# Optimization experiments

Hardware: AMD Instinct MI355X
Metric: run time of the kernel (lower is better)

## Reference

```python
import jax, jax.numpy as jnp
import numpy as np

B, T, C, H = 32, 576, 1024, 16
D = C // H  # head_dim = 64

def setup_inputs() -> dict:
    key = jax.random.key(0)
    ks = jax.random.split(key, 5)
    s = 1.0 / np.sqrt(C)
    return {
        "emb_img": jax.random.normal(ks[0], (B, T, C), dtype=jnp.float32),
        "w_qkv": jax.random.normal(ks[1], (C, 3 * C), dtype=jnp.float32) * s,
        "b_qkv": jnp.zeros((3 * C,), dtype=jnp.float32),
        "w_proj": jax.random.normal(ks[2], (C, C), dtype=jnp.float32) * s,
        "b_proj": jnp.zeros((C,), dtype=jnp.float32),
    }

def reference(emb_img, w_qkv, b_qkv, w_proj, b_proj):
    # fused QKV projection
    qkv = emb_img @ w_qkv + b_qkv                       # [B,T,3C]
    q, k, v = jnp.split(qkv, 3, axis=-1)                # each [B,T,C]
    def heads(x):
        return x.reshape(B, T, H, D).transpose(0, 2, 1, 3)  # [B,H,T,D]
    q, k, v = heads(q), heads(k), heads(v)
    # note: original scales by 1/head_dim (not 1/sqrt(head_dim))
    scores = jnp.einsum("bhqd,bhkd->bhqk", q, k) * (1.0 / D)
    causal = jnp.tril(jnp.ones((T, T), dtype=bool))
    scores = jnp.where(causal[None, None], scores, -jnp.inf)
    att = jax.nn.softmax(scores, axis=-1)               # [B,H,T,T]
    y = jnp.einsum("bhqk,bhkd->bhqd", att, v)           # [B,H,T,D]
    y = y.transpose(0, 2, 1, 3).reshape(B, T, C)
    return y @ w_proj + b_proj
```

## Files before the change

kernel.cpp:

```cpp
#include <hip/hip_runtime.h>
#include <stdint.h>

namespace {

constexpr int kB = 32, kT = 576, kC = 1024, kH = 16, kD = 64;
constexpr int kM = kB * kT;
constexpr int kNqkv = 3 * kC;
constexpr float kQScale = 1.4426950408889634f / 64.0f;

typedef uint16_t u16;
typedef __attribute__((ext_vector_type(4))) float f32x4;
typedef __attribute__((ext_vector_type(8))) short short8;
typedef __attribute__((ext_vector_type(8))) __bf16 bf16x8;
typedef __attribute__((ext_vector_type(4))) uint16_t u16x4;

#define VMCNT(n) asm volatile("s_waitcnt vmcnt(" #n ")" ::: "memory")

__device__ __forceinline__ float fexp2(float x) {
  return __builtin_amdgcn_exp2f(x);
}

__device__ __forceinline__ f32x4 mfma_bf16(short8 a, short8 b, f32x4 c) {
  return __builtin_amdgcn_mfma_f32_16x16x32_bf16(
      __builtin_bit_cast(bf16x8, a), __builtin_bit_cast(bf16x8, b), c, 0, 0, 0);
}

__device__ __forceinline__ u16 to_bf16(float x) {
  uint32_t u = __float_as_uint(x);
  u += 0x7fffu + ((u >> 16) & 1u);
  return (u16)(u >> 16);
}

__device__ __forceinline__ void gload_lds16(const void* g, void* l) {
  __builtin_amdgcn_global_load_lds(
      (const __attribute__((address_space(1))) uint32_t*)(uintptr_t)g,
      (__attribute__((address_space(3))) uint32_t*)(uintptr_t)l,
      16, 0, 0);
}

__device__ __forceinline__ void bar() {
  asm volatile("" ::: "memory");
  __builtin_amdgcn_s_barrier();
  asm volatile("" ::: "memory");
}

__global__ __launch_bounds__(256) void cvt_bf16_kernel(
    const float* __restrict__ in, u16* __restrict__ out, int n4) {
  const int i = blockIdx.x * 256 + threadIdx.x;
  if (i >= n4) return;
  const f32x4 v = ((const f32x4*)in)[i];
  u16x4 o;
#pragma unroll
  for (int j = 0; j < 4; ++j) o[j] = to_bf16(v[j]);
  ((u16x4*)out)[i] = o;
}

__global__ void tconv_kernel(const float* __restrict__ in, u16* __restrict__ out,
                             int K, int N) {
  __shared__ u16 tile[32][33];
  const int nb = blockIdx.x * 32;
  const int kb = blockIdx.y * 32;
  const int tx = threadIdx.x;
  const int ty = threadIdx.y;
#pragma unroll
  for (int i = 0; i < 32; i += 8)
    tile[ty + i][tx] = to_bf16(in[(size_t)(kb + ty + i) * N + nb + tx]);
  __syncthreads();
#pragma unroll
  for (int i = 0; i < 32; i += 8)
    out[(size_t)(nb + ty + i) * K + kb + tx] = tile[tx][ty + i];
}

__global__ __launch_bounds__(512, 4) void gemm_qkv(
    const u16* __restrict__ A, const u16* __restrict__ Bt,
    const float* __restrict__ bias,
    u16* __restrict__ outQ, u16* __restrict__ outK, u16* __restrict__ outVT) {
  constexpr int Kc = 1024;
  constexpr int NT = Kc / 32;
  __shared__ char lds[2][24576];

  const int tid = threadIdx.x;
  const int wave = tid >> 6;
  const int lane = tid & 63;
  const int lo = lane & 15;
  const int hi = lane >> 4;
  const int wr = wave >> 1;
  const int wc = wave & 1;

  const int lin = blockIdx.x + blockIdx.y * 24;
  const int l2 = (lin & 7) * 216 + (lin >> 3);
  const int n0 = (l2 % 24) * 128;
  const int m0 = (l2 / 24) * 256;

  const u16* srcA[2];
#pragma unroll
  for (int c = 0; c < 2; ++c) {
    const int off = c * 8192 + tid * 16;
    const int p = off >> 7;
    const int col = (off & 127) ^ ((p & 7) << 4);
    const int Ar = (col < 64) ? p : p + 128;
    const int k_ = (col & 63) >> 1;
    srcA[c] = A + (size_t)(m0 + Ar) * Kc + k_;
  }
  const u16* srcB1;
  {
    const int off = tid * 16;
    const int p = off >> 7;
    const int col = (off & 127) ^ ((p & 7) << 4);
    const int Br = (col < 64) ? p : p + 64;
    const int k_ = (col & 63) >> 1;
    srcB1 = Bt + (size_t)(n0 + Br) * Kc + k_;
  }

  auto stage = [&](int slot, int t) {
    char* base = &lds[slot][0];
    gload_lds16(srcA[0] + t * 32, base + tid * 16);
    gload_lds16(srcA[1] + t * 32, base + 8192 + tid * 16);
    gload_lds16(srcB1 + t * 32, base + 16384 + tid * 16);
  };

  f32x4 acc[4][4] = {};

  auto compute = [&](int slot) {
    const char* base = &lds[slot][0];
    const char* baseB = base + 16384;
    const int swz = (lo & 7) << 4;
    short8 af[4], bf[4];
#pragma unroll
    for (int i = 0; i < 4; ++i) {
      const int row = wr * 64 + i * 16 + lo;
      const int prow = row & 127;
      const int half = row >> 7;
      af[i] = *(const short8*)(base + prow * 128 + ((half * 64 + hi * 16) ^ swz));
    }
#pragma unroll
    for (int j = 0; j < 4; ++j) {
      const int row = wc * 64 + j * 16 + lo;
      const int prow = row & 63;
      const int half = row >> 6;
      bf[j] = *(const short8*)(baseB + prow * 128 + ((half * 64 + hi * 16) ^ swz));
    }
    __builtin_amdgcn_s_setprio(1);
#pragma unroll
    for (int i = 0; i < 4; ++i)
#pragma unroll
      for (int j = 0; j < 4; ++j)
        acc[i][j] = mfma_bf16(af[i], bf[j], acc[i][j]);
    __builtin_amdgcn_s_setprio(0);
  };

  stage(0, 0);
  for (int t = 0; t < NT; ++t) {
    if (t + 1 < NT) {
      stage((t + 1) & 1, t + 1);
      VMCNT(3);
    } else {
      VMCNT(0);
    }
    bar();
    compute(t & 1);
    bar();
  }

  if (n0 >= 2048) {
    u16* wlds = (u16*)&lds[0][0] + wave * (32 * 66);
    uint32_t* wlds32 = (uint32_t*)wlds;
#pragma unroll
    for (int jp = 0; jp < 2; ++jp) {
#pragma unroll
      for (int jj = 0; jj < 2; ++jj) {
        const int j = jp * 2 + jj;
        const int n = n0 + wc * 64 + j * 16 + lo;
        const float bv = bias[n];
        const int dl = jj * 16 + lo;
#pragma unroll
        for (int i = 0; i < 4; ++i)
#pragma unroll
          for (int rp = 0; rp < 2; ++rp) {
            const u16 w0 = to_bf16(acc[i][j][rp * 2] + bv);
            const u16 w1 = to_bf16(acc[i][j][rp * 2 + 1] + bv);
            wlds32[dl * 33 + i * 8 + hi * 2 + rp] =
                (uint32_t)w0 | ((uint32_t)w1 << 16);
          }
      }
#pragma unroll
      for (int p = 0; p < 8; ++p) {
        const int dl32 = p * 4 + hi;
        const int n = n0 + wc * 64 + jp * 32 + dl32;
        const int c = n & 1023;
        const int hh = c >> 6;
        const int d = c & 63;
        const int m = m0 + wr * 64 + lo * 4;
        const int bb = m / kT;
        const int t = m - bb * kT;
        const u16x4 v = *(const u16x4*)&wlds[dl32 * 66 + lo * 4];
        *(u16x4*)&outVT[((size_t)(bb * kH + hh) * kD + d) * kT + t] = v;
      }
    }
  } else {
#pragma unroll
    for (int j = 0; j < 4; ++j) {
      const int n = n0 + wc * 64 + j * 16 + lo;
      const float bv = bias[n];
      const int which = n >> 10;
      const int c = n & 1023;
      const int hh = c >> 6;
      const int d = c & 63;
#pragma unroll
      for (int i = 0; i < 4; ++i) {
        const int mrow = m0 + wr * 64 + i * 16 + hi * 4;
#pragma unroll
        for (int r = 0; r < 4; ++r) {
          const int m = mrow + r;
          const int bb = m / kT;
          const int t = m - bb * kT;
          const float v = acc[i][j][r] + bv;
          if (which == 0)
            outQ[((size_t)(bb * kH + hh) * kT + t) * kD + d] = to_bf16(v * kQScale);
          else
            outK[((size_t)(bb * kH + hh) * kT + t) * kD + d] = to_bf16(v);
        }
      }
    }
  }
}

__global__ __launch_bounds__(256, 3) void gemm_proj(
    const u16* __restrict__ A, const u16* __restrict__ Bt,
    const float* __restrict__ bias, float* __restrict__ outF) {
  constexpr int Kc = 1024;
  constexpr int NT = Kc / 32;
  __shared__ char lds[3][16384];

  const int tid = threadIdx.x;
  const int wave = tid >> 6;
  const int lane = tid & 63;
  const int lo = lane & 15;
  const int hi = lane >> 4;
  const int wr = wave >> 1;
  const int wc = wave & 1;

  const int lin = blockIdx.x + blockIdx.y * 8;
  const int l2 = (lin & 7) * 144 + (lin >> 3);
  const int n0 = (l2 & 7) * 128;
  const int m0 = (l2 >> 3) * 128;

  const u16* srcA[2];
  const u16* srcB[2];
#pragma unroll
  for (int c = 0; c < 2; ++c) {
    const int off = c * 4096 + tid * 16;
    const int p = off >> 7;
    const int col = (off & 127) ^ ((p & 7) << 4);
    const int r_ = (col < 64) ? p : p + 64;
    const int k_ = (col & 63) >> 1;
    srcA[c] = A + (size_t)(m0 + r_) * Kc + k_;
    srcB[c] = Bt + (size_t)(n0 + r_) * Kc + k_;
  }

  auto stage = [&](int slot, int t) {
    char* base = &lds[slot][0];
#pragma unroll
    for (int c = 0; c < 2; ++c) {
      gload_lds16(srcA[c] + t * 32, base + c * 4096 + wave * 1024);
      gload_lds16(srcB[c] + t * 32, base + 8192 + c * 4096 + wave * 1024);
    }
  };

  f32x4 acc[4][4] = {};

  auto compute = [&](int slot) {
    const char* base = &lds[slot][0];
    const char* baseB = base + 8192;
    const int swz = (lo & 7) << 4;
    short8 af[4], bf[4];
#pragma unroll
    for (int i = 0; i < 4; ++i)
      af[i] = *(const short8*)(base + (i * 16 + lo) * 128 + ((wr * 64 + hi * 16) ^ swz));
#pragma unroll
    for (int j = 0; j < 4; ++j)
      bf[j] = *(const short8*)(baseB + (j * 16 + lo) * 128 + ((wc * 64 + hi * 16) ^ swz));
    __builtin_amdgcn_s_setprio(1);
#pragma unroll
    for (int i = 0; i < 4; ++i)
#pragma unroll
      for (int j = 0; j < 4; ++j)
        acc[i][j] = mfma_bf16(af[i], bf[j], acc[i][j]);
    __builtin_amdgcn_s_setprio(0);
  };

  stage(0, 0);
  stage(1, 1);
  for (int t = 0; t < NT - 2; ++t) {
    stage((t + 2) % 3, t + 2);
    VMCNT(8);
    bar();
    compute(t % 3);
    bar();
  }
  VMCNT(4);
  bar();
  compute((NT - 2) % 3);
  bar();
  VMCNT(0);
  bar();
  compute((NT - 1) % 3);

#pragma unroll
  for (int j = 0; j < 4; ++j) {
    const int n = n0 + wc * 64 + j * 16 + lo;
    const float bv = bias[n];
#pragma unroll
    for (int i = 0; i < 4; ++i) {
      const int mrow = m0 + wr * 64 + i * 16 + hi * 4;
#pragma unroll
      for (int r = 0; r < 4; ++r)
        outF[(size_t)(mrow + r) * kC + n] = acc[i][j][r] + bv;
    }
  }
}

__global__ __launch_bounds__(256) void attn_kernel(
    const u16* __restrict__ Q, const u16* __restrict__ K,
    const u16* __restrict__ VT, u16* __restrict__ Y) {
  __shared__ u16 P[4][32][72];

  const int idx = blockIdx.x;
  const int qi = 4 - (idx >> 9);
  const int bh = idx & 511;
  const int wave = threadIdx.x >> 6;
  const int lane = threadIdx.x & 63;
  const int lo = lane & 15;
  const int hi = lane >> 4;
  const int q0 = qi * 128 + wave * 32;
  if (q0 >= kT) return;

  const u16* Qb = Q + (size_t)bh * kT * kD;
  const u16* Kb = K + (size_t)bh * kT * kD;
  const u16* Vb = VT + (size_t)bh * kD * kT;

  short8 qf[2][2];
#pragma unroll
  for (int h = 0; h < 2; ++h) {
    const u16* qp = Qb + (q0 + h * 16 + lo) * kD + hi * 8;
    qf[h][0] = *(const short8*)qp;
    qf[h][1] = *(const short8*)(qp + 32);
  }

  f32x4 acc[2][4] = {};
  float mrun[2] = {-3e38f, -3e38f};
  float lsum[2] = {0.f, 0.f};

  short8 kf[4][2];
#pragma unroll
  for (int kc = 0; kc < 4; ++kc) {
    const u16* kp = Kb + (kc * 16 + lo) * kD + hi * 8;
    kf[kc][0] = *(const short8*)kp;
    kf[kc][1] = *(const short8*)(kp + 32);
  }

  const int kv_end = q0 + 32;
  for (int kv = 0; kv < kv_end; kv += 64) {
    f32x4 s[2][4];
#pragma unroll
    for (int kc = 0; kc < 4; ++kc)
#pragma unroll
      for (int h = 0; h < 2; ++h) {
        f32x4 z = {0.f, 0.f, 0.f, 0.f};
        z = mfma_bf16(kf[kc][0], qf[h][0], z);
        z = mfma_bf16(kf[kc][1], qf[h][1], z);
        s[h][kc] = z;
      }
    short8 vf[4][2];
#pragma unroll
    for (int nt = 0; nt < 4; ++nt) {
      const u16* vp = Vb + (nt * 16 + lo) * kT + kv + hi * 8;
      vf[nt][0] = *(const short8*)vp;
      vf[nt][1] = *(const short8*)(vp + 32);
    }
    if (kv + 64 < kv_end) {
#pragma unroll
      for (int kc = 0; kc < 4; ++kc) {
        const u16* kp = Kb + (kv + 64 + kc * 16 + lo) * kD + hi * 8;
        kf[kc][0] = *(const short8*)kp;
        kf[kc][1] = *(const short8*)(kp + 32);
      }
    }
    if (kv + 63 > q0) {
#pragma unroll
      for (int h = 0; h < 2; ++h) {
        const int q = q0 + h * 16 + lo;
#pragma unroll
        for (int kc = 0; kc < 4; ++kc)
#pragma unroll
          for (int r = 0; r < 4; ++r)
            if (kv + kc * 16 + hi * 4 + r > q) s[h][kc][r] = -3e38f;
      }
    }
#pragma unroll
    for (int h = 0; h < 2; ++h) {
      float m01 = fmaxf(fmaxf(s[h][0][0], s[h][0][1]), fmaxf(s[h][0][2], s[h][0][3]));
      float m23 = fmaxf(fmaxf(s[h][1][0], s[h][1][1]), fmaxf(s[h][1][2], s[h][1][3]));
      float m45 = fmaxf(fmaxf(s[h][2][0], s[h][2][1]), fmaxf(s[h][2][2], s[h][2][3]));
      float m67 = fmaxf(fmaxf(s[h][3][0], s[h][3][1]), fmaxf(s[h][3][2], s[h][3][3]));
      float pm = fmaxf(fmaxf(m01, m23), fmaxf(m45, m67));
      pm = fmaxf(pm, __shfl_xor(pm, 16));
      pm = fmaxf(pm, __shfl_xor(pm, 32));
      const float mnew = fmaxf(mrun[h], pm);
      const float corr = fexp2(mrun[h] - mnew);
      mrun[h] = mnew;
      float psum = 0.f;
#pragma unroll
      for (int kc = 0; kc < 4; ++kc) {
        u16x4 pk;
#pragma unroll
        for (int r = 0; r < 4; ++r) {
          const float pv = fexp2(s[h][kc][r] - mnew);
          psum += pv;
          pk[r] = to_bf16(pv);
        }
        *(u16x4*)&P[wave][h * 16 + lo][kc * 16 + hi * 4] = pk;
      }
      lsum[h] = lsum[h] * corr + psum;
#pragma unroll
      for (int nt = 0; nt < 4; ++nt)
#pragma unroll
        for (int r = 0; r < 4; ++r) acc[h][nt][r] *= corr;
    }
    short8 pf[2][2];
#pragma unroll
    for (int h = 0; h < 2; ++h) {
      pf[h][0] = *(const short8*)&P[wave][h * 16 + lo][hi * 8];
      pf[h][1] = *(const short8*)&P[wave][h * 16 + lo][32 + hi * 8];
    }
#pragma unroll
    for (int nt = 0; nt < 4; ++nt)
#pragma unroll
      for (int h = 0; h < 2; ++h) {
        acc[h][nt] = mfma_bf16(pf[h][0], vf[nt][0], acc[h][nt]);
        acc[h][nt] = mfma_bf16(pf[h][1], vf[nt][1], acc[h][nt]);
      }
  }

#pragma unroll
  for (int h = 0; h < 2; ++h) {
    lsum[h] += __shfl_xor(lsum[h], 16);
    lsum[h] += __shfl_xor(lsum[h], 32);
  }
  const int b = bh >> 4, hh = bh & 15;
#pragma unroll
  for (int h = 0; h < 2; ++h)
#pragma unroll
    for (int r = 0; r < 4; ++r) {
      const float linv = 1.0f / __shfl(lsum[h], hi * 4 + r);
      const int t = q0 + h * 16 + hi * 4 + r;
      const size_t base = ((size_t)(b * kT + t) * kH + hh) * kD;
#pragma unroll
      for (int nt = 0; nt < 4; ++nt)
        Y[base + nt * 16 + lo] = to_bf16(acc[h][nt][r] * linv);
    }
}

}

extern "C" void kernel_launch(void* const* d_in, const int* in_sizes, int n_in,
                              void* d_out, int out_size, void* d_ws, size_t ws_size,
                              hipStream_t stream) {
  (void)in_sizes; (void)n_in; (void)out_size; (void)ws_size;
  const float* emb   = (const float*)d_in[0];
  const float* wqkv  = (const float*)d_in[1];
  const float* bqkv  = (const float*)d_in[2];
  const float* wproj = (const float*)d_in[3];
  const float* bproj = (const float*)d_in[4];
  float* out = (float*)d_out;

  char* p = (char*)d_ws;
  u16* embb   = (u16*)p; p += (size_t)kM * kC * 2;
  u16* wqkvt  = (u16*)p; p += (size_t)kNqkv * kC * 2;
  u16* wprojt = (u16*)p; p += (size_t)kC * kC * 2;
  u16* Qh     = (u16*)p; p += (size_t)kM * kC * 2;
  u16* Kh     = (u16*)p; p += (size_t)kM * kC * 2;
  u16* VTh    = (u16*)p; p += (size_t)kM * kC * 2;
  u16* Yh     = (u16*)p; p += (size_t)kM * kC * 2;

  const int n4 = kM * kC / 4;
  cvt_bf16_kernel<<<dim3((n4 + 255) / 256), 256, 0, stream>>>(emb, embb, n4);
  tconv_kernel<<<dim3(kNqkv / 32, kC / 32), dim3(32, 8), 0, stream>>>(wqkv, wqkvt, kC, kNqkv);
  tconv_kernel<<<dim3(kC / 32, kC / 32), dim3(32, 8), 0, stream>>>(wproj, wprojt, kC, kC);
  gemm_qkv<<<dim3(kNqkv / 128, kM / 256), 512, 0, stream>>>(
      embb, wqkvt, bqkv, Qh, Kh, VTh);
  attn_kernel<<<dim3(5 * kB * kH), 256, 0, stream>>>(Qh, Kh, VTh, Yh);
  gemm_proj<<<dim3(kC / 128, kM / 128), 256, 0, stream>>>(
      Yh, wprojt, bproj, out);
}
```

Baseline: 317.7 us.

## Enlarge proj GEMM tile to 256x128 and skip masked half-tiles in attention

The output projection GEMM now uses 512-thread blocks with 256x128 tiles, double-buffered LDS instead of triple-buffered, so each B tile is reused across twice as many rows. The attention kernel splits the KV loop into unmasked full tiles and one masked diagonal tile, and for the last tile it processes only the 32 needed keys when the query block ends mid-tile. This cuts wasted MFMA, exp and mask work on the causal diagonal. The cost is shallower pipelining in the GEMM and higher per-block register and LDS pressure.

```diff
diff --git a/kernel.cpp b/kernel.cpp
--- a/kernel.cpp
+++ b/kernel.cpp
@@ -225,12 +225,12 @@
   }
 }
 
-__global__ __launch_bounds__(256, 3) void gemm_proj(
+__global__ __launch_bounds__(512, 4) void gemm_proj(
     const u16* __restrict__ A, const u16* __restrict__ Bt,
     const float* __restrict__ bias, float* __restrict__ outF) {
   constexpr int Kc = 1024;
   constexpr int NT = Kc / 32;
-  __shared__ char lds[3][16384];
+  __shared__ char lds[2][24576];
 
   const int tid = threadIdx.x;
   const int wave = tid >> 6;
@@ -241,45 +241,58 @@
   const int wc = wave & 1;
 
   const int lin = blockIdx.x + blockIdx.y * 8;
-  const int l2 = (lin & 7) * 144 + (lin >> 3);
-  const int n0 = (l2 & 7) * 128;
-  const int m0 = (l2 >> 3) * 128;
+  const int l2 = (lin & 7) * 72 + (lin >> 3);
+  const int n0 = (l2 % 8) * 128;
+  const int m0 = (l2 / 8) * 256;
 
   const u16* srcA[2];
-  const u16* srcB[2];
 #pragma unroll
   for (int c = 0; c < 2; ++c) {
-    const int off = c * 4096 + tid * 16;
+    const int off = c * 8192 + tid * 16;
     const int p = off >> 7;
     const int col = (off & 127) ^ ((p & 7) << 4);
-    const int r_ = (col < 64) ? p : p + 64;
+    const int Ar = (col < 64) ? p : p + 128;
     const int k_ = (col & 63) >> 1;
-    srcA[c] = A + (size_t)(m0 + r_) * Kc + k_;
-    srcB[c] = Bt + (size_t)(n0 + r_) * Kc + k_;
+    srcA[c] = A + (size_t)(m0 + Ar) * Kc + k_;
+  }
+  const u16* srcB1;
+  {
+    const int off = tid * 16;
+    const int p = off >> 7;
+    const int col = (off & 127) ^ ((p & 7) << 4);
+    const int Br = (col < 64) ? p : p + 64;
+    const int k_ = (col & 63) >> 1;
+    srcB1 = Bt + (size_t)(n0 + Br) * Kc + k_;
   }
 
   auto stage = [&](int slot, int t) {
     char* base = &lds[slot][0];
-#pragma unroll
-    for (int c = 0; c < 2; ++c) {
-      gload_lds16(srcA[c] + t * 32, base + c * 4096 + wave * 1024);
-      gload_lds16(srcB[c] + t * 32, base + 8192 + c * 4096 + wave * 1024);
-    }
+    gload_lds16(srcA[0] + t * 32, base + tid * 16);
+    gload_lds16(srcA[1] + t * 32, base + 8192 + tid * 16);
+    gload_lds16(srcB1 + t * 32, base + 16384 + tid * 16);
   };
 
   f32x4 acc[4][4] = {};
 
   auto compute = [&](int slot) {
     const char* base = &lds[slot][0];
-    const char* baseB = base + 8192;
+    const char* baseB = base + 16384;
     const int swz = (lo & 7) << 4;
     short8 af[4], bf[4];
 #pragma unroll
-    for (int i = 0; i < 4; ++i)
-      af[i] = *(const short8*)(base + (i * 16 + lo) * 128 + ((wr * 64 + hi * 16) ^ swz));
-#pragma unroll
-    for (int j = 0; j < 4; ++j)
-      bf[j] = *(const short8*)(baseB + (j * 16 + lo) * 128 + ((wc * 64 + hi * 16) ^ swz));
+    for (int i = 0; i < 4; ++i) {
+      const int row = wr * 64 + i * 16 + lo;
+      const int prow = row & 127;
+      const int half = row >> 7;
+      af[i] = *(const short8*)(base + prow * 128 + ((half * 64 + hi * 16) ^ swz));
+    }
+#pragma unroll
+    for (int j = 0; j < 4; ++j) {
+      const int row = wc * 64 + j * 16 + lo;
+      const int prow = row & 63;
+      const int half = row >> 6;
+      bf[j] = *(const short8*)(baseB + prow * 128 + ((half * 64 + hi * 16) ^ swz));
+    }
     __builtin_amdgcn_s_setprio(1);
 #pragma unroll
     for (int i = 0; i < 4; ++i)
@@ -290,21 +303,17 @@
   };
 
   stage(0, 0);
-  stage(1, 1);
-  for (int t = 0; t < NT - 2; ++t) {
-    stage((t + 2) % 3, t + 2);
-    VMCNT(8);
+  for (int t = 0; t < NT; ++t) {
+    if (t + 1 < NT) {
+      stage((t + 1) & 1, t + 1);
+      VMCNT(3);
+    } else {
+      VMCNT(0);
+    }
     bar();
-    compute(t % 3);
+    compute(t & 1);
     bar();
   }
-  VMCNT(4);
-  bar();
-  compute((NT - 2) % 3);
-  bar();
-  VMCNT(0);
-  bar();
-  compute((NT - 1) % 3);
 
 #pragma unroll
   for (int j = 0; j < 4; ++j) {
@@ -359,51 +368,77 @@
     kf[kc][1] = *(const short8*)(kp + 32);
   }
 
-  const int kv_end = q0 + 32;
-  for (int kv = 0; kv < kv_end; kv += 64) {
+  const int nfull = q0 >> 6;
+  const bool tail4 = ((q0 >> 5) & 1) != 0;
+
+  auto do_tile = [&](int kv, int kclim, bool masked, bool have_next,
+                     bool next_wide) {
     f32x4 s[2][4];
 #pragma unroll
-    for (int kc = 0; kc < 4; ++kc)
-#pragma unroll
-      for (int h = 0; h < 2; ++h) {
-        f32x4 z = {0.f, 0.f, 0.f, 0.f};
-        z = mfma_bf16(kf[kc][0], qf[h][0], z);
-        z = mfma_bf16(kf[kc][1], qf[h][1], z);
-        s[h][kc] = z;
-      }
+    for (int kc = 0; kc < 4; ++kc) {
+      if (kc < kclim) {
+#pragma unroll
+        for (int h = 0; h < 2; ++h) {
+          f32x4 z = {0.f, 0.f, 0.f, 0.f};
+          z = mfma_bf16(kf[kc][0], qf[h][0], z);
+          z = mfma_bf16(kf[kc][1], qf[h][1], z);
+          s[h][kc] = z;
+        }
+      }
+    }
     short8 vf[4][2];
 #pragma unroll
     for (int nt = 0; nt < 4; ++nt) {
       const u16* vp = Vb + (nt * 16 + lo) * kT + kv + hi * 8;
       vf[nt][0] = *(const short8*)vp;
-      vf[nt][1] = *(const short8*)(vp + 32);
-    }
-    if (kv + 64 < kv_end) {
-#pragma unroll
-      for (int kc = 0; kc < 4; ++kc) {
+      if (kclim == 4) vf[nt][1] = *(const short8*)(vp + 32);
+    }
+    if (have_next) {
+#pragma unroll
+      for (int kc = 0; kc < 2; ++kc) {
         const u16* kp = Kb + (kv + 64 + kc * 16 + lo) * kD + hi * 8;
         kf[kc][0] = *(const short8*)kp;
         kf[kc][1] = *(const short8*)(kp + 32);
       }
-    }
-    if (kv + 63 > q0) {
+      if (next_wide) {
+#pragma unroll
+        for (int kc = 2; kc < 4; ++kc) {
+          const u16* kp = Kb + (kv + 64 + kc * 16 + lo) * kD + hi * 8;
+          kf[kc][0] = *(const short8*)kp;
+          kf[kc][1] = *(const short8*)(kp + 32);
+        }
+      }
+    }
+    if (masked) {
 #pragma unroll
       for (int h = 0; h < 2; ++h) {
         const int q = q0 + h * 16 + lo;
 #pragma unroll
         for (int kc = 0; kc < 4; ++kc)
-#pragma unroll
-          for (int r = 0; r < 4; ++r)
-            if (kv + kc * 16 + hi * 4 + r > q) s[h][kc][r] = -3e38f;
+          if (kc < kclim) {
+#pragma unroll
+            for (int r = 0; r < 4; ++r)
+              if (kv + kc * 16 + hi * 4 + r > q) s[h][kc][r] = -3e38f;
+          }
       }
     }
 #pragma unroll
     for (int h = 0; h < 2; ++h) {
-      float m01 = fmaxf(fmaxf(s[h][0][0], s[h][0][1]), fmaxf(s[h][0][2], s[h][0][3]));
-      float m23 = fmaxf(fmaxf(s[h][1][0], s[h][1][1]), fmaxf(s[h][1][2], s[h][1][3]));
-      float m45 = fmaxf(fmaxf(s[h][2][0], s[h][2][1]), fmaxf(s[h][2][2], s[h][2][3]));
-      float m67 = fmaxf(fmaxf(s[h][3][0], s[h][3][1]), fmaxf(s[h][3][2], s[h][3][3]));
-      float pm = fmaxf(fmaxf(m01, m23), fmaxf(m45, m67));
+      float pm;
+      {
+        float m01 = fmaxf(fmaxf(s[h][0][0], s[h][0][1]),
+                          fmaxf(s[h][0][2], s[h][0][3]));
+        float m23 = fmaxf(fmaxf(s[h][1][0], s[h][1][1]),
+                          fmaxf(s[h][1][2], s[h][1][3]));
+        pm = fmaxf(m01, m23);
+        if (kclim == 4) {
+          float m45 = fmaxf(fmaxf(s[h][2][0], s[h][2][1]),
+                            fmaxf(s[h][2][2], s[h][2][3]));
+          float m67 = fmaxf(fmaxf(s[h][3][0], s[h][3][1]),
+                            fmaxf(s[h][3][2], s[h][3][3]));
+          pm = fmaxf(pm, fmaxf(m45, m67));
+        }
+      }
       pm = fmaxf(pm, __shfl_xor(pm, 16));
       pm = fmaxf(pm, __shfl_xor(pm, 32));
       const float mnew = fmaxf(mrun[h], pm);
@@ -411,36 +446,37 @@
       mrun[h] = mnew;
       float psum = 0.f;
 #pragma unroll
-      for (int kc = 0; kc < 4; ++kc) {
-        u16x4 pk;
-#pragma unroll
-        for (int r = 0; r < 4; ++r) {
-          const float pv = fexp2(s[h][kc][r] - mnew);
-          psum += pv;
-          pk[r] = to_bf16(pv);
+      for (int kc = 0; kc < 4; ++kc)
+        if (kc < kclim) {
+          u16x4 pk;
+#pragma unroll
+          for (int r = 0; r < 4; ++r) {
+            const float pv = fexp2(s[h][kc][r] - mnew);
+            psum += pv;
+            pk[r] = to_bf16(pv);
+          }
+          *(u16x4*)&P[wave][h * 16 + lo][kc * 16 + hi * 4] = pk;
         }
-        *(u16x4*)&P[wave][h * 16 + lo][kc * 16 + hi * 4] = pk;
-      }
       lsum[h] = lsum[h] * corr + psum;
 #pragma unroll
       for (int nt = 0; nt < 4; ++nt)
 #pragma unroll
         for (int r = 0; r < 4; ++r) acc[h][nt][r] *= corr;
-    }
-    short8 pf[2][2];
-#pragma unroll
-    for (int h = 0; h < 2; ++h) {
-      pf[h][0] = *(const short8*)&P[wave][h * 16 + lo][hi * 8];
-      pf[h][1] = *(const short8*)&P[wave][h * 16 + lo][32 + hi * 8];
-    }
-#pragma unroll
-    for (int nt = 0; nt < 4; ++nt)
-#pragma unroll
-      for (int h = 0; h < 2; ++h) {
-        acc[h][nt] = mfma_bf16(pf[h][0], vf[nt][0], acc[h][nt]);
-        acc[h][nt] = mfma_bf16(pf[h][1], vf[nt][1], acc[h][nt]);
-      }
-  }
+      const short8 pf0 = *(const short8*)&P[wave][h * 16 + lo][hi * 8];
+      short8 pf1;
+      if (kclim == 4) pf1 = *(const short8*)&P[wave][h * 16 + lo][32 + hi * 8];
+#pragma unroll
+      for (int nt = 0; nt < 4; ++nt) {
+        acc[h][nt] = mfma_bf16(pf0, vf[nt][0], acc[h][nt]);
+        if (kclim == 4) acc[h][nt] = mfma_bf16(pf1, vf[nt][1], acc[h][nt]);
+      }
+    }
+  };
+
+  for (int it = 0; it < nfull; ++it)
+    do_tile(it * 64, 4, false, true, (it + 1 < nfull) || tail4);
+  if (tail4) do_tile(nfull * 64, 4, true, false, false);
+  else       do_tile(nfull * 64, 2, true, false, false);
 
 #pragma unroll
   for (int h = 0; h < 2; ++h) {
@@ -490,6 +526,6 @@
   gemm_qkv<<<dim3(kNqkv / 128, kM / 256), 512, 0, stream>>>(
       embb, wqkvt, bqkv, Qh, Kh, VTh);
   attn_kernel<<<dim3(5 * kB * kH), 256, 0, stream>>>(Qh, Kh, VTh, Yh);
-  gemm_proj<<<dim3(kC / 128, kM / 128), 256, 0, stream>>>(
+  gemm_proj<<<dim3(kC / 128, kM / 256), 512, 0, stream>>>(
       Yh, wprojt, bproj, out);
 }
```

Measured after the change: 316.1 us, median of 2. About the same (-0.5%).
